# Optimization experiments

Measured on AMD Instinct MI355X. Metric: run time of the kernel, lower is better.

The kernel has to match this reference:

```python
import jax, jax.numpy as jnp
import numpy as np

HIDDEN = 128
IN = 2
OUT = 2

def setup_inputs() -> dict:
    key = jax.random.key(0)
    ks = jax.random.split(key, 12)
    B, S = 1024, 512
    s_ih = 1.0 / np.sqrt(HIDDEN)
    return {
        "x0": jax.random.normal(ks[0], (B, OUT), jnp.float32),
        "v_seq": jax.random.normal(ks[1], (B, S, IN), jnp.float32),
        # GRU params (PyTorch layout: gates ordered r, z, n)
        "W_ih": jax.random.uniform(ks[2], (3 * HIDDEN, IN), jnp.float32, -s_ih, s_ih),
        "W_hh": jax.random.uniform(ks[3], (3 * HIDDEN, HIDDEN), jnp.float32, -s_ih, s_ih),
        "b_ih": jax.random.uniform(ks[4], (3 * HIDDEN,), jnp.float32, -s_ih, s_ih),
        "b_hh": jax.random.uniform(ks[5], (3 * HIDDEN,), jnp.float32, -s_ih, s_ih),
        # output Linear hidden -> OUT
        "W_out": jax.random.uniform(ks[6], (OUT, HIDDEN), jnp.float32, -s_ih, s_ih),
        "b_out": jax.random.uniform(ks[7], (OUT,), jnp.float32, -s_ih, s_ih),
        # residual predictor: Linear(OUT+IN -> HIDDEN//2), ReLU, Linear(-> OUT)
        "W_r1": jax.random.uniform(ks[8], (HIDDEN // 2, OUT + IN), jnp.float32, -0.5, 0.5),
        "b_r1": jax.random.uniform(ks[9], (HIDDEN // 2,), jnp.float32, -0.5, 0.5),
        "W_r2": jax.random.uniform(ks[10], (OUT, HIDDEN // 2), jnp.float32, -s_ih, s_ih),
        "b_r2": jax.random.uniform(ks[11], (OUT,), jnp.float32, -s_ih, s_ih),
    }

def _gru_seq(v_seq, W_ih, W_hh, b_ih, b_hh):
    B, S, _ = v_seq.shape
    H = W_hh.shape[1]
    # precompute input projections for all timesteps: [B,S,3H]
    xp = jnp.einsum('bsi,gi->bsg', v_seq, W_ih) + b_ih
    xp = jnp.swapaxes(xp, 0, 1)  # [S,B,3H]

    def step(h, xp_t):
        gh = h @ W_hh.T + b_hh  # [B,3H]
        xr, xz, xn = jnp.split(xp_t, 3, axis=-1)
        hr, hz, hn = jnp.split(gh, 3, axis=-1)
        r = jax.nn.sigmoid(xr + hr)
        z = jax.nn.sigmoid(xz + hz)
        n = jnp.tanh(xn + r * hn)
        h_new = (1.0 - z) * n + z * h
        return h_new, h_new

    h0 = jnp.zeros((B, H), v_seq.dtype)
    _, h_seq = jax.lax.scan(step, h0, xp)
    return jnp.swapaxes(h_seq, 0, 1)  # [B,S,H]

def reference(x0, v_seq, W_ih, W_hh, b_ih, b_hh, W_out, b_out, W_r1, b_r1, W_r2, b_r2):
    h_seq = _gru_seq(v_seq, W_ih, W_hh, b_ih, b_hh)
    x_pred = jnp.einsum('bsh,oh->bso', h_seq, W_out) + b_out  # [B,S,OUT]
    # In the torch loop, x_prev at step t is x0 for t=0 else x_pred[:,t-1],
    # so the loop vectorizes as a shift along time.
    x_prev = jnp.concatenate([x0[:, None, :], x_pred[:, :-1, :]], axis=1)
    # input_size == output_size, so v_t[:, :OUT] == v_t (no padding branch)
    ri = jnp.concatenate([x_prev, v_seq], axis=-1)  # [B,S,OUT+IN]
    hid = jax.nn.relu(jnp.einsum('bsf,hf->bsh', ri, W_r1) + b_r1)
    residual = jnp.einsum('bsh,oh->bso', hid, W_r2) + b_r2
    physics_pred = x_prev + v_seq + residual
    physics_violations = x_pred - physics_pred
    return (x_pred, physics_violations)
```

## Files before the change

kernel.cpp:

```cpp
#include <hip/hip_runtime.h>
#include <stdint.h>

#define BB 1024
#define SS 512
#define HH 128
#define MM 4
#define BLK 512
#define NBLK (BB / MM)
#define HPS 136
#define RS 32
#define RStr 144

typedef float f32x4 __attribute__((ext_vector_type(4)));
typedef float f32x2 __attribute__((ext_vector_type(2)));
typedef _Float16 f16x8 __attribute__((ext_vector_type(8)));

#define LO_SCALE 2048.0f
#define LO_INV   (1.0f / 2048.0f)

__device__ __forceinline__ float sigf(float x) { return 1.0f / (1.0f + __expf(-x)); }
__device__ __forceinline__ float tanh_fast(float x) { return 2.0f / (1.0f + __expf(-2.0f * x)) - 1.0f; }

__global__ __launch_bounds__(BLK, 2) void pig_kernel(
    const float* __restrict__ x0, const float* __restrict__ v_seq,
    const float* __restrict__ W_ih, const float* __restrict__ W_hh,
    const float* __restrict__ b_ih, const float* __restrict__ b_hh,
    const float* __restrict__ W_out, const float* __restrict__ b_out,
    const float* __restrict__ W_r1, const float* __restrict__ b_r1,
    const float* __restrict__ W_r2, const float* __restrict__ b_r2,
    float* __restrict__ out)
{
    __shared__ __align__(16) _Float16 hpack[2][16 * HPS];
    __shared__ __align__(16) _Float16 ring[RS * 4 * RStr];
    __shared__ __align__(16) float    v_lds[SS * 8];
    __shared__ __align__(16) float    xs[RS + 1][8];
    __shared__ __align__(16) float    wpk[64][8];
    __shared__ float xc[2][8];

    const int tid  = threadIdx.x;
    const int wave = tid >> 6;
    const int lane = tid & 63;
    const int quad = lane >> 4;
    const int col  = lane & 15;
    const int row0 = blockIdx.x * MM;
    const int j    = wave * 16 + col;

    f16x8 whi[3][4];
#pragma unroll
    for (int nt = 0; nt < 3; ++nt) {
        const int g = nt * HH + j;
#pragma unroll
        for (int kk = 0; kk < 4; ++kk) {
            const float* p = W_hh + g * HH + kk * 32 + quad * 8;
            f16x8 fh;
#pragma unroll
            for (int i = 0; i < 8; ++i) fh[i] = (_Float16)p[i];
            whi[nt][kk] = fh;
        }
    }

    const float wr0 = W_ih[j*2],        wr1 = W_ih[j*2+1];
    const float wz0 = W_ih[(HH+j)*2],   wz1 = W_ih[(HH+j)*2+1];
    const float wn0 = W_ih[(2*HH+j)*2], wn1 = W_ih[(2*HH+j)*2+1];
    const float br  = b_ih[j]      + b_hh[j];
    const float bz  = b_ih[HH+j]   + b_hh[HH+j];
    const float bni = b_ih[2*HH+j];
    const float bnh = b_hh[2*HH+j];

    const int g8  = tid >> 3;
    const int l8  = tid & 7;
    const int oA  = g8 & 1;
    const int mA  = (g8 >> 1) & 3;
    const int tt8 = g8 >> 3;
    float woA[16];
#pragma unroll
    for (int i = 0; i < 16; ++i) woA[i] = W_out[oA * HH + l8 * 16 + i];
    const float boA = b_out[oA];

    const int qB = tid & 3;
    const int mB = (tid >> 2) & 3;
    const int tB = tid >> 4;
    const float b2B = b_r2[qB & 1];

    for (int idx = tid; idx < 2 * 16 * HPS; idx += BLK) ((_Float16*)hpack)[idx] = (_Float16)0.0f;
    for (int idx = tid; idx < MM * SS * 2; idx += BLK) {
        const int m = idx >> 10, i = idx & 1023;
        v_lds[(i >> 1) * 8 + m * 2 + (i & 1)] = v_seq[(size_t)(row0 + m) * (SS * 2) + i];
    }
    if (tid < 64) {
        wpk[tid][0] = W_r1[tid*4];   wpk[tid][1] = W_r1[tid*4+1];
        wpk[tid][2] = W_r1[tid*4+2]; wpk[tid][3] = W_r1[tid*4+3];
        wpk[tid][4] = b_r1[tid];
        wpk[tid][5] = W_r2[tid];     wpk[tid][6] = W_r2[64 + tid];
        wpk[tid][7] = 0.0f;
    }
    if (tid < 8)
        xc[0][tid] = x0[(size_t)(row0 + (tid >> 1)) * 2 + (tid & 1)];
    __syncthreads();

    float hold = 0.0f;
    for (int t = 0; t < SS; ++t) {
        const int cur = t & 1, nxt = cur ^ 1;

        f32x4 aH0 = {0,0,0,0}, aH1 = {0,0,0,0}, aH2 = {0,0,0,0};
#pragma unroll
        for (int kk = 0; kk < 4; ++kk) {
            f16x8 af = *(const f16x8*)&hpack[cur][col * HPS + kk * 32 + quad * 8];
            aH0 = __builtin_amdgcn_mfma_f32_16x16x32_f16(af, whi[0][kk], aH0, 0, 0, 0);
            aH1 = __builtin_amdgcn_mfma_f32_16x16x32_f16(af, whi[1][kk], aH1, 0, 0, 0);
            aH2 = __builtin_amdgcn_mfma_f32_16x16x32_f16(af, whi[2][kk], aH2, 0, 0, 0);
        }
        const float gh0 = aH0[0] + aH0[1] * LO_INV;
        const float gh1 = aH1[0] + aH1[1] * LO_INV;
        const float gh2 = aH2[0] + aH2[1] * LO_INV;

        const f32x2 vv2 = *(const f32x2*)&v_lds[t * 8 + quad * 2];
        const float r = sigf(gh0 + vv2[0]*wr0 + vv2[1]*wr1 + br);
        const float z = sigf(gh1 + vv2[0]*wz0 + vv2[1]*wz1 + bz);
        const float n = tanh_fast(vv2[0]*wn0 + vv2[1]*wn1 + bni + r * (gh2 + bnh));
        hold = n + z * (hold - n);

        const _Float16 hh = (_Float16)hold;
        hpack[nxt][(4*quad)     * HPS + j] = hh;
        hpack[nxt][(4*quad + 1) * HPS + j] = (_Float16)((hold - (float)hh) * LO_SCALE);
        ring[((t & (RS-1)) * 4 + quad) * RStr + j] = hh;

        __syncthreads();

        if ((t & (RS - 1)) == (RS - 1)) {
            const int f  = t >> 5;
            const int t0 = t - (RS - 1);

            if (tid < 8) xs[0][tid] = xc[f & 1][tid];
#pragma unroll
            for (int p = 0; p < 4; ++p) {
                const int tt = p * 8 + tt8;
                const f16x8 h0 = *(const f16x8*)&ring[(tt * 4 + mA) * RStr + l8 * 16];
                const f16x8 h1 = *(const f16x8*)&ring[(tt * 4 + mA) * RStr + l8 * 16 + 8];
                float acc = 0.0f;
#pragma unroll
                for (int i = 0; i < 8; ++i) {
                    acc += (float)h0[i] * woA[i];
                    acc += (float)h1[i] * woA[8 + i];
                }
                acc += __shfl_xor(acc, 1, 64);
                acc += __shfl_xor(acc, 2, 64);
                acc += __shfl_xor(acc, 4, 64);
                if (l8 == 0) xs[1 + tt][mA * 2 + oA] = acc + boA;
            }
            __syncthreads();

            {
                const float xp0 = xs[tB][mB*2], xp1 = xs[tB][mB*2+1];
                const f32x2 vt2 = *(const f32x2*)&v_lds[(t0 + tB) * 8 + mB * 2];
                float rss0 = 0.0f, rss1 = 0.0f;
#pragma unroll
                for (int uu = 0; uu < 16; ++uu) {
                    const int u = qB * 16 + uu;
                    const f32x4 wA = *(const f32x4*)&wpk[u][0];
                    const f32x4 wB = *(const f32x4*)&wpk[u][4];
                    const float hu = fmaxf(wB[0] + wA[0]*xp0 + wA[1]*xp1 + wA[2]*vt2[0] + wA[3]*vt2[1], 0.0f);
                    rss0 += hu * wB[1];
                    rss1 += hu * wB[2];
                }
                rss0 += __shfl_xor(rss0, 1, 64);
                rss1 += __shfl_xor(rss1, 1, 64);
                rss0 += __shfl_xor(rss0, 2, 64);
                rss1 += __shfl_xor(rss1, 2, 64);
                if (qB < 2) {
                    const int o = qB;
                    const float xpred = xs[tB + 1][mB*2 + o];
                    const float xpv   = xs[tB][mB*2 + o];
                    const float vv    = v_lds[(t0 + tB) * 8 + mB*2 + o];
                    const float resid = (o ? rss1 : rss0) + b2B;
                    const float viol  = xpred - (xpv + vv + resid);
                    const size_t base = (size_t)(row0 + mB) * (SS * 2) + (t0 + tB) * 2 + o;
                    out[base] = xpred;
                    out[(size_t)BB * SS * 2 + base] = viol;
                }
                if (tid < 8) xc[(f + 1) & 1][tid] = xs[RS][tid];
            }
            __syncthreads();
        }
    }
}

extern "C" void kernel_launch(void* const* d_in, const int* in_sizes, int n_in,
                              void* d_out, int out_size, void* d_ws, size_t ws_size,
                              hipStream_t stream) {
    pig_kernel<<<dim3(NBLK), dim3(BLK), 0, stream>>>(
        (const float*)d_in[0],  (const float*)d_in[1],  (const float*)d_in[2],
        (const float*)d_in[3],  (const float*)d_in[4],  (const float*)d_in[5],
        (const float*)d_in[6],  (const float*)d_in[7],  (const float*)d_in[8],
        (const float*)d_in[9],  (const float*)d_in[10], (const float*)d_in[11],
        (float*)d_out);
}
```

Before: 394.9 us.

## Split batch across twice as many blocks, each wave computing two hidden tiles

Halves the batch rows per block from 4 to 2 and the block size from 512 to 256 threads, doubling the grid so two independent blocks can share a CU. Each wave now covers 32 hidden units, so it holds twice the W_hh fragments and issues six MFMAs per k-slice instead of three. The intent is to shorten each per-step barrier across fewer waves and let two blocks' serial recurrences interleave, hiding latency. In exchange, the MFMA M dimension is less used (only 2 rows plus their lo parts), half the lanes sit idle in the gate math, and register pressure rises from the doubled weight fragments.

```diff
diff --git a/kernel.cpp b/kernel.cpp
--- a/kernel.cpp
+++ b/kernel.cpp
@@ -4,12 +4,12 @@
 #define BB 1024
 #define SS 512
 #define HH 128
-#define MM 4
-#define BLK 512
+#define MM 2
+#define BLK 256
 #define NBLK (BB / MM)
 #define HPS 136
 #define RS 32
-#define RStr 144
+#define RStr 160
 
 typedef float f32x4 __attribute__((ext_vector_type(4)));
 typedef float f32x2 __attribute__((ext_vector_type(2)));
@@ -31,11 +31,11 @@
     float* __restrict__ out)
 {
     __shared__ __align__(16) _Float16 hpack[2][16 * HPS];
-    __shared__ __align__(16) _Float16 ring[RS * 4 * RStr];
-    __shared__ __align__(16) float    v_lds[SS * 8];
-    __shared__ __align__(16) float    xs[RS + 1][8];
+    __shared__ __align__(16) _Float16 ring[RS * MM * RStr];
+    __shared__ __align__(16) float    v_lds[SS * 4];
+    __shared__ __align__(16) float    xs[RS + 1][4];
     __shared__ __align__(16) float    wpk[64][8];
-    __shared__ float xc[2][8];
+    __shared__ float xc[2][4];
 
     const int tid  = threadIdx.x;
     const int wave = tid >> 6;
@@ -43,49 +43,56 @@
     const int quad = lane >> 4;
     const int col  = lane & 15;
     const int row0 = blockIdx.x * MM;
-    const int j    = wave * 16 + col;
-
-    f16x8 whi[3][4];
-#pragma unroll
-    for (int nt = 0; nt < 3; ++nt) {
-        const int g = nt * HH + j;
-#pragma unroll
-        for (int kk = 0; kk < 4; ++kk) {
-            const float* p = W_hh + g * HH + kk * 32 + quad * 8;
-            f16x8 fh;
-#pragma unroll
-            for (int i = 0; i < 8; ++i) fh[i] = (_Float16)p[i];
-            whi[nt][kk] = fh;
-        }
-    }
-
-    const float wr0 = W_ih[j*2],        wr1 = W_ih[j*2+1];
-    const float wz0 = W_ih[(HH+j)*2],   wz1 = W_ih[(HH+j)*2+1];
-    const float wn0 = W_ih[(2*HH+j)*2], wn1 = W_ih[(2*HH+j)*2+1];
-    const float br  = b_ih[j]      + b_hh[j];
-    const float bz  = b_ih[HH+j]   + b_hh[HH+j];
-    const float bni = b_ih[2*HH+j];
-    const float bnh = b_hh[2*HH+j];
+
+    f16x8 whi[3][2][4];
+#pragma unroll
+    for (int nt = 0; nt < 3; ++nt)
+#pragma unroll
+        for (int jg = 0; jg < 2; ++jg) {
+            const int g = nt * HH + wave * 32 + jg * 16 + col;
+#pragma unroll
+            for (int kk = 0; kk < 4; ++kk) {
+                const float* p = W_hh + g * HH + kk * 32 + quad * 8;
+                f16x8 fh;
+#pragma unroll
+                for (int i = 0; i < 8; ++i) fh[i] = (_Float16)p[i];
+                whi[nt][jg][kk] = fh;
+            }
+        }
+
+    const int mG = quad & 1;
+    float wih[2][6], bg[2][4];
+#pragma unroll
+    for (int jg = 0; jg < 2; ++jg) {
+        const int j = wave * 32 + jg * 16 + col;
+        wih[jg][0] = W_ih[j*2];          wih[jg][1] = W_ih[j*2+1];
+        wih[jg][2] = W_ih[(HH+j)*2];     wih[jg][3] = W_ih[(HH+j)*2+1];
+        wih[jg][4] = W_ih[(2*HH+j)*2];   wih[jg][5] = W_ih[(2*HH+j)*2+1];
+        bg[jg][0]  = b_ih[j]      + b_hh[j];
+        bg[jg][1]  = b_ih[HH+j]   + b_hh[HH+j];
+        bg[jg][2]  = b_ih[2*HH+j];
+        bg[jg][3]  = b_hh[2*HH+j];
+    }
 
     const int g8  = tid >> 3;
     const int l8  = tid & 7;
     const int oA  = g8 & 1;
-    const int mA  = (g8 >> 1) & 3;
-    const int tt8 = g8 >> 3;
+    const int mA  = (g8 >> 1) & 1;
+    const int tt8 = g8 >> 2;
     float woA[16];
 #pragma unroll
     for (int i = 0; i < 16; ++i) woA[i] = W_out[oA * HH + l8 * 16 + i];
     const float boA = b_out[oA];
 
     const int qB = tid & 3;
-    const int mB = (tid >> 2) & 3;
-    const int tB = tid >> 4;
+    const int mB = (tid >> 2) & 1;
+    const int tB = tid >> 3;
     const float b2B = b_r2[qB & 1];
 
     for (int idx = tid; idx < 2 * 16 * HPS; idx += BLK) ((_Float16*)hpack)[idx] = (_Float16)0.0f;
     for (int idx = tid; idx < MM * SS * 2; idx += BLK) {
         const int m = idx >> 10, i = idx & 1023;
-        v_lds[(i >> 1) * 8 + m * 2 + (i & 1)] = v_seq[(size_t)(row0 + m) * (SS * 2) + i];
+        v_lds[(i >> 1) * 4 + m * 2 + (i & 1)] = v_seq[(size_t)(row0 + m) * (SS * 2) + i];
     }
     if (tid < 64) {
         wpk[tid][0] = W_r1[tid*4];   wpk[tid][1] = W_r1[tid*4+1];
@@ -94,36 +101,60 @@
         wpk[tid][5] = W_r2[tid];     wpk[tid][6] = W_r2[64 + tid];
         wpk[tid][7] = 0.0f;
     }
-    if (tid < 8)
+    if (tid < MM*2)
         xc[0][tid] = x0[(size_t)(row0 + (tid >> 1)) * 2 + (tid & 1)];
     __syncthreads();
 
-    float hold = 0.0f;
+    float hold0 = 0.0f, hold1 = 0.0f;
     for (int t = 0; t < SS; ++t) {
         const int cur = t & 1, nxt = cur ^ 1;
 
-        f32x4 aH0 = {0,0,0,0}, aH1 = {0,0,0,0}, aH2 = {0,0,0,0};
+        f32x4 a00 = {0,0,0,0}, a01 = {0,0,0,0};
+        f32x4 a10 = {0,0,0,0}, a11 = {0,0,0,0};
+        f32x4 a20 = {0,0,0,0}, a21 = {0,0,0,0};
 #pragma unroll
         for (int kk = 0; kk < 4; ++kk) {
             f16x8 af = *(const f16x8*)&hpack[cur][col * HPS + kk * 32 + quad * 8];
-            aH0 = __builtin_amdgcn_mfma_f32_16x16x32_f16(af, whi[0][kk], aH0, 0, 0, 0);
-            aH1 = __builtin_amdgcn_mfma_f32_16x16x32_f16(af, whi[1][kk], aH1, 0, 0, 0);
-            aH2 = __builtin_amdgcn_mfma_f32_16x16x32_f16(af, whi[2][kk], aH2, 0, 0, 0);
-        }
-        const float gh0 = aH0[0] + aH0[1] * LO_INV;
-        const float gh1 = aH1[0] + aH1[1] * LO_INV;
-        const float gh2 = aH2[0] + aH2[1] * LO_INV;
-
-        const f32x2 vv2 = *(const f32x2*)&v_lds[t * 8 + quad * 2];
-        const float r = sigf(gh0 + vv2[0]*wr0 + vv2[1]*wr1 + br);
-        const float z = sigf(gh1 + vv2[0]*wz0 + vv2[1]*wz1 + bz);
-        const float n = tanh_fast(vv2[0]*wn0 + vv2[1]*wn1 + bni + r * (gh2 + bnh));
-        hold = n + z * (hold - n);
-
-        const _Float16 hh = (_Float16)hold;
-        hpack[nxt][(4*quad)     * HPS + j] = hh;
-        hpack[nxt][(4*quad + 1) * HPS + j] = (_Float16)((hold - (float)hh) * LO_SCALE);
-        ring[((t & (RS-1)) * 4 + quad) * RStr + j] = hh;
+            a00 = __builtin_amdgcn_mfma_f32_16x16x32_f16(af, whi[0][0][kk], a00, 0, 0, 0);
+            a01 = __builtin_amdgcn_mfma_f32_16x16x32_f16(af, whi[0][1][kk], a01, 0, 0, 0);
+            a10 = __builtin_amdgcn_mfma_f32_16x16x32_f16(af, whi[1][0][kk], a10, 0, 0, 0);
+            a11 = __builtin_amdgcn_mfma_f32_16x16x32_f16(af, whi[1][1][kk], a11, 0, 0, 0);
+            a20 = __builtin_amdgcn_mfma_f32_16x16x32_f16(af, whi[2][0][kk], a20, 0, 0, 0);
+            a21 = __builtin_amdgcn_mfma_f32_16x16x32_f16(af, whi[2][1][kk], a21, 0, 0, 0);
+        }
+
+        if (quad < 2) {
+            const f32x2 vv2 = *(const f32x2*)&v_lds[t * 4 + mG * 2];
+            const float v0 = vv2[0], v1 = vv2[1];
+
+            const float gr0 = a00[0] + a00[1] * LO_INV;
+            const float gz0 = a10[0] + a10[1] * LO_INV;
+            const float gn0 = a20[0] + a20[1] * LO_INV;
+            const float r0g = sigf(gr0 + v0*wih[0][0] + v1*wih[0][1] + bg[0][0]);
+            const float z0g = sigf(gz0 + v0*wih[0][2] + v1*wih[0][3] + bg[0][1]);
+            const float n0g = tanh_fast(v0*wih[0][4] + v1*wih[0][5] + bg[0][2] + r0g * (gn0 + bg[0][3]));
+            hold0 = n0g + z0g * (hold0 - n0g);
+
+            const float gr1 = a01[0] + a01[1] * LO_INV;
+            const float gz1 = a11[0] + a11[1] * LO_INV;
+            const float gn1 = a21[0] + a21[1] * LO_INV;
+            const float r1g = sigf(gr1 + v0*wih[1][0] + v1*wih[1][1] + bg[1][0]);
+            const float z1g = sigf(gz1 + v0*wih[1][2] + v1*wih[1][3] + bg[1][1]);
+            const float n1g = tanh_fast(v0*wih[1][4] + v1*wih[1][5] + bg[1][2] + r1g * (gn1 + bg[1][3]));
+            hold1 = n1g + z1g * (hold1 - n1g);
+
+            const int j0 = wave * 32 + col;
+            const int j1 = j0 + 16;
+            const _Float16 hh0 = (_Float16)hold0;
+            const _Float16 hh1 = (_Float16)hold1;
+            hpack[nxt][(4*mG)     * HPS + j0] = hh0;
+            hpack[nxt][(4*mG + 1) * HPS + j0] = (_Float16)((hold0 - (float)hh0) * LO_SCALE);
+            hpack[nxt][(4*mG)     * HPS + j1] = hh1;
+            hpack[nxt][(4*mG + 1) * HPS + j1] = (_Float16)((hold1 - (float)hh1) * LO_SCALE);
+            const int rbase = ((t & (RS-1)) * MM + mG) * RStr;
+            ring[rbase + j0] = hh0;
+            ring[rbase + j1] = hh1;
+        }
 
         __syncthreads();
 
@@ -131,12 +162,12 @@
             const int f  = t >> 5;
             const int t0 = t - (RS - 1);
 
-            if (tid < 8) xs[0][tid] = xc[f & 1][tid];
+            if (tid < MM*2) xs[0][tid] = xc[f & 1][tid];
 #pragma unroll
             for (int p = 0; p < 4; ++p) {
                 const int tt = p * 8 + tt8;
-                const f16x8 h0 = *(const f16x8*)&ring[(tt * 4 + mA) * RStr + l8 * 16];
-                const f16x8 h1 = *(const f16x8*)&ring[(tt * 4 + mA) * RStr + l8 * 16 + 8];
+                const f16x8 h0 = *(const f16x8*)&ring[(tt * MM + mA) * RStr + l8 * 16];
+                const f16x8 h1 = *(const f16x8*)&ring[(tt * MM + mA) * RStr + l8 * 16 + 8];
                 float acc = 0.0f;
 #pragma unroll
                 for (int i = 0; i < 8; ++i) {
@@ -152,7 +183,7 @@
 
             {
                 const float xp0 = xs[tB][mB*2], xp1 = xs[tB][mB*2+1];
-                const f32x2 vt2 = *(const f32x2*)&v_lds[(t0 + tB) * 8 + mB * 2];
+                const f32x2 vt2 = *(const f32x2*)&v_lds[(t0 + tB) * 4 + mB * 2];
                 float rss0 = 0.0f, rss1 = 0.0f;
 #pragma unroll
                 for (int uu = 0; uu < 16; ++uu) {
@@ -171,14 +202,14 @@
                     const int o = qB;
                     const float xpred = xs[tB + 1][mB*2 + o];
                     const float xpv   = xs[tB][mB*2 + o];
-                    const float vv    = v_lds[(t0 + tB) * 8 + mB*2 + o];
+                    const float vv    = v_lds[(t0 + tB) * 4 + mB*2 + o];
                     const float resid = (o ? rss1 : rss0) + b2B;
                     const float viol  = xpred - (xpv + vv + resid);
                     const size_t base = (size_t)(row0 + mB) * (SS * 2) + (t0 + tB) * 2 + o;
                     out[base] = xpred;
                     out[(size_t)BB * SS * 2 + base] = viol;
                 }
-                if (tid < 8) xc[(f + 1) & 1][tid] = xs[RS][tid];
+                if (tid < MM*2) xc[(f + 1) & 1][tid] = xs[RS][tid];
             }
             __syncthreads();
         }
```

Measured after the change: 606.5 us. 1.54x slower.
